# Performance work log

Hardware: AMD Instinct MI355X
Metric: run time of the kernel (lower is better)

Reference implementation:

```python
import jax, jax.numpy as jnp
import numpy as np

B, T, F = 32, 500, 640   # batch, encoder frames, encoder feature dim
H = 640                  # prediction-net LSTM hidden
J = 640                  # joint dim
V = 1024                 # vocab size
BLANK = 0                # blank_id


def setup_inputs() -> dict:
    key = jax.random.key(0)
    ks = jax.random.split(key, 8)
    s = 0.02
    return {
        "tn_output": jax.random.normal(ks[0], (B, T, F), jnp.float32),
        "E": jax.random.normal(ks[1], (V, H), jnp.float32) * s,        # prediction-net embedding
        "W_ih": jax.random.normal(ks[2], (H, 4 * H), jnp.float32) * s,  # LSTM input weights
        "W_hh": jax.random.normal(ks[3], (H, 4 * H), jnp.float32) * s,  # LSTM recurrent weights
        "b_lstm": jnp.zeros((4 * H,), jnp.float32),
        "W_enc": jax.random.normal(ks[4], (F, J), jnp.float32) * s,     # joint: encoder projection
        "W_dec": jax.random.normal(ks[5], (H, J), jnp.float32) * s,     # joint: decoder projection
        "b_j": jnp.zeros((J,), jnp.float32),
        "W_out": jax.random.normal(ks[6], (J, V), jnp.float32) * s,     # joint: output projection
        "b_out": jnp.zeros((V,), jnp.float32),
    }


def _lstm_step(x, h, c, W_ih, W_hh, b):
    gates = x @ W_ih + h @ W_hh + b  # [B, 4H]
    i, f, g, o = jnp.split(gates, 4, axis=-1)
    c2 = jax.nn.sigmoid(f) * c + jax.nn.sigmoid(i) * jnp.tanh(g)
    h2 = jax.nn.sigmoid(o) * jnp.tanh(c2)
    return h2, c2


def _greedy_decode(tn_output, E, W_ih, W_hh, b_lstm, W_enc, W_dec, b_j, W_out, b_out):
    Bc = tn_output.shape[0]
    dt = tn_output.dtype
    tok0 = jnp.full((Bc,), BLANK, jnp.int32)
    h0 = jnp.zeros((Bc, H), dt)
    c0 = jnp.zeros((Bc, H), dt)
    # initial decoder call on blank token (hidden=None -> zeros)
    h1, c1 = _lstm_step(E[tok0], h0, c0, W_ih, W_hh, b_lstm)
    g0 = h1  # out_PN

    def step(carry, enc_t):
        h, c, g, last_tok, scores = carry
        # joint network + log_softmax (idempotent, applied once)
        logits = jnp.tanh(enc_t @ W_enc + g @ W_dec + b_j) @ W_out + b_out  # [B, V]
        logp = jax.nn.log_softmax(logits, axis=-1)
        tok = jnp.argmax(logp, axis=-1)                                     # [B]
        lp = jnp.take_along_axis(logp, tok[:, None], axis=1)[:, 0]          # logp_targets
        emit = tok != BLANK                                                 # [B] bool
        scores = scores + jnp.where(emit, lp, jnp.zeros_like(lp))
        new_tok = jnp.where(emit, tok.astype(jnp.int32), last_tok)
        # conditional decoder step: run LSTM on all rows, keep updates only where emit
        h2, c2 = _lstm_step(E[new_tok], h, c, W_ih, W_hh, b_lstm)
        m = emit[:, None]
        h = jnp.where(m, h2, h)
        c = jnp.where(m, c2, c)
        g = jnp.where(m, h2, g)
        out_tok = jnp.where(emit, tok.astype(jnp.int32), jnp.int32(BLANK))
        return (h, c, g, new_tok, scores), out_tok

    init = (h1, c1, g0, tok0, jnp.zeros((Bc,), dt))
    (_, _, _, _, scores), toks = jax.lax.scan(step, init, jnp.swapaxes(tn_output, 0, 1))
    return jnp.swapaxes(toks, 0, 1), scores  # [B,T] int tokens (BLANK = no emission), [B] logp scores


def reference(tn_output, E, W_ih, W_hh, b_lstm, W_enc, W_dec, b_j, W_out, b_out):
    toks, scores = _greedy_decode(tn_output, E, W_ih, W_hh, b_lstm, W_enc, W_dec, b_j, W_out, b_out)
    # original returns (predictions, mean of exp(logp_scores), None, None)
    return toks, jnp.exp(scores).mean()
```

## Files before the change

### kernel.cpp

```cpp
#include <hip/hip_runtime.h>
#include <math.h>

#define BB 32
#define TT 500
#define HH 640
#define VV 1024
#define NWG 100

typedef float f32x4 __attribute__((ext_vector_type(4)));
typedef float f32x2 __attribute__((ext_vector_type(2)));
typedef unsigned int u32x2 __attribute__((ext_vector_type(2)));


__device__ __forceinline__ float sigf(float x) { return 1.0f / (1.0f + expf(-x)); }

__device__ __forceinline__ unsigned int fkey(float x) {
    unsigned int u = __float_as_uint(x);
    return (u & 0x80000000u) ? ~u : (u | 0x80000000u);
}

__device__ __forceinline__ unsigned long long shflxor_u64(unsigned long long v, int m) {
    unsigned int lo = (unsigned int)v, hi = (unsigned int)(v >> 32);
    lo = (unsigned int)__shfl_xor((int)lo, m);
    hi = (unsigned int)__shfl_xor((int)hi, m);
    return ((unsigned long long)hi << 32) | lo;
}

__device__ __forceinline__ void stg1_sc(float* p, float v) {
    asm volatile("global_store_dword %0, %1, off sc0 sc1" :: "v"(p), "v"(v) : "memory");
}
__device__ __forceinline__ void stg4_sc(float* p, f32x4 v) {
    asm volatile("global_store_dwordx4 %0, %1, off sc0 sc1" :: "v"(p), "v"(v) : "memory");
}
__device__ __forceinline__ void stg2u_sc(unsigned long long* p, unsigned long long v) {
    u32x2 uv; uv.x = (unsigned int)v; uv.y = (unsigned int)(v >> 32);
    asm volatile("global_store_dwordx2 %0, %1, off sc0 sc1" :: "v"(p), "v"(uv) : "memory");
}

__device__ __forceinline__ void stage_rows(const float* src, float* dst) {
    f32x4 t0,t1,t2,t3,t4,t5,t6,t7,t8,t9,t10,t11,t12,t13,t14,t15,t16,t17,t18,t19;
    asm volatile(
        "global_load_dwordx4 %0,  %20, off sc0 sc1\n\t"
        "global_load_dwordx4 %1,  %20, off offset:16 sc0 sc1\n\t"
        "global_load_dwordx4 %2,  %20, off offset:32 sc0 sc1\n\t"
        "global_load_dwordx4 %3,  %20, off offset:48 sc0 sc1\n\t"
        "global_load_dwordx4 %4,  %20, off offset:64 sc0 sc1\n\t"
        "global_load_dwordx4 %5,  %20, off offset:80 sc0 sc1\n\t"
        "global_load_dwordx4 %6,  %20, off offset:96 sc0 sc1\n\t"
        "global_load_dwordx4 %7,  %20, off offset:112 sc0 sc1\n\t"
        "global_load_dwordx4 %8,  %20, off offset:128 sc0 sc1\n\t"
        "global_load_dwordx4 %9,  %20, off offset:144 sc0 sc1\n\t"
        "global_load_dwordx4 %10, %20, off offset:160 sc0 sc1\n\t"
        "global_load_dwordx4 %11, %20, off offset:176 sc0 sc1\n\t"
        "global_load_dwordx4 %12, %20, off offset:192 sc0 sc1\n\t"
        "global_load_dwordx4 %13, %20, off offset:208 sc0 sc1\n\t"
        "global_load_dwordx4 %14, %20, off offset:224 sc0 sc1\n\t"
        "global_load_dwordx4 %15, %20, off offset:240 sc0 sc1\n\t"
        "global_load_dwordx4 %16, %20, off offset:256 sc0 sc1\n\t"
        "global_load_dwordx4 %17, %20, off offset:272 sc0 sc1\n\t"
        "global_load_dwordx4 %18, %20, off offset:288 sc0 sc1\n\t"
        "global_load_dwordx4 %19, %20, off offset:304 sc0 sc1\n\t"
        "s_waitcnt vmcnt(0)"
        : "=&v"(t0),"=&v"(t1),"=&v"(t2),"=&v"(t3),"=&v"(t4),"=&v"(t5),"=&v"(t6),"=&v"(t7),
          "=&v"(t8),"=&v"(t9),"=&v"(t10),"=&v"(t11),"=&v"(t12),"=&v"(t13),"=&v"(t14),"=&v"(t15),
          "=&v"(t16),"=&v"(t17),"=&v"(t18),"=&v"(t19)
        : "v"(src) : "memory");
    f32x4* d = (f32x4*)dst;
    d[0]=t0; d[1]=t1; d[2]=t2; d[3]=t3; d[4]=t4; d[5]=t5; d[6]=t6; d[7]=t7;
    d[8]=t8; d[9]=t9; d[10]=t10; d[11]=t11; d[12]=t12; d[13]=t13; d[14]=t14;
    d[15]=t15; d[16]=t16; d[17]=t17; d[18]=t18; d[19]=t19;
}

__device__ __forceinline__ void gbar(unsigned int* arrive, unsigned int* release,
                                     int w, int tid, unsigned int k) {
    asm volatile("s_waitcnt vmcnt(0)" ::: "memory");
    __syncthreads();
    if (w == 0) {
        if (tid > 0 && tid < NWG)
            while (__hip_atomic_load(&arrive[tid * 32], __ATOMIC_RELAXED,
                                     __HIP_MEMORY_SCOPE_AGENT) < k)
                __builtin_amdgcn_s_sleep(2);
        __syncthreads();
        if (tid > 0 && tid < NWG)
            __hip_atomic_store(&release[tid * 32], k, __ATOMIC_RELAXED,
                               __HIP_MEMORY_SCOPE_AGENT);
    } else {
        if (tid == 0) {
            __hip_atomic_store(&arrive[w * 32], k, __ATOMIC_RELAXED,
                               __HIP_MEMORY_SCOPE_AGENT);
            while (__hip_atomic_load(&release[w * 32], __ATOMIC_RELAXED,
                                     __HIP_MEMORY_SCOPE_AGENT) < k)
                __builtin_amdgcn_s_sleep(2);
        }
        __syncthreads();
    }
}

__global__ __launch_bounds__(256) void gemm_bias_kernel(
    const float* __restrict__ A, const float* __restrict__ Bm,
    const float* __restrict__ bias, float* __restrict__ C,
    int M, int N, int K)
{
    __shared__ float As[16][65];
    __shared__ float Bs[16][64];
    int tid = threadIdx.x;
    int m0 = blockIdx.y * 64, n0 = blockIdx.x * 64;
    int ar = tid >> 2, ac = (tid & 3) * 4;
    int br4 = (tid >> 6) * 4, bc = tid & 63;
    int ty = tid >> 4, tx = tid & 15;
    float acc[4][4] = {};
    for (int k0 = 0; k0 < K; k0 += 16) {
        float4 av = *(const float4*)(A + (long)(m0 + ar) * K + k0 + ac);
        As[ac + 0][ar] = av.x; As[ac + 1][ar] = av.y;
        As[ac + 2][ar] = av.z; As[ac + 3][ar] = av.w;
#pragma unroll
        for (int i = 0; i < 4; ++i)
            Bs[br4 + i][bc] = Bm[(long)(k0 + br4 + i) * N + n0 + bc];
        __syncthreads();
#pragma unroll
        for (int kk = 0; kk < 16; ++kk) {
            float a[4], b[4];
#pragma unroll
            for (int i = 0; i < 4; ++i) a[i] = As[kk][ty * 4 + i];
#pragma unroll
            for (int j = 0; j < 4; ++j) b[j] = Bs[kk][tx * 4 + j];
#pragma unroll
            for (int i = 0; i < 4; ++i)
#pragma unroll
                for (int j = 0; j < 4; ++j)
                    acc[i][j] = fmaf(a[i], b[j], acc[i][j]);
        }
        __syncthreads();
    }
#pragma unroll
    for (int i = 0; i < 4; ++i)
#pragma unroll
        for (int j = 0; j < 4; ++j)
            C[(long)(m0 + ty * 4 + i) * N + n0 + tx * 4 + j] =
                acc[i][j] + bias[n0 + tx * 4 + j];
}

__global__ void transpose_cat_kernel(const float* __restrict__ Wdec,
                                     const float* __restrict__ Whh,
                                     float* __restrict__ WcatT)
{
    int c = blockIdx.x;
    const float* src; long stride;
    if (c < 640) { src = Wdec + c; stride = 640; }
    else         { src = Whh + (c - 640); stride = 2560; }
    for (int k = threadIdx.x; k < 640; k += 256)
        WcatT[(long)c * 640 + k] = src[(long)k * stride];
}

__global__ void transpose_out_kernel(const float* __restrict__ Wout,
                                     float* __restrict__ WoT)
{
    int v = blockIdx.x;
    for (int k = threadIdx.x; k < 640; k += 256)
        WoT[(long)v * 640 + k] = Wout[(long)k * 1024 + v];
}

__global__ void init_kernel(const float* __restrict__ EW, float* __restrict__ h,
                            float* __restrict__ c, float* __restrict__ scores,
                            unsigned int* __restrict__ arrive,
                            unsigned int* __restrict__ release,
                            unsigned long long* __restrict__ pmax,
                            float* __restrict__ psum)
{
    int tid = threadIdx.x;
    for (int j = tid; j < HH; j += 256) {
        float gi = EW[j], gg = EW[1280 + j], go = EW[1920 + j];
        float c1 = sigf(gi) * tanhf(gg);
        float h1 = sigf(go) * tanhf(c1);
        for (int b = 0; b < BB; ++b) { h[b * 640 + j] = h1; c[b * 640 + j] = c1; }
    }
    if (tid < 32) scores[tid] = 0.f;
    if (tid < NWG) { arrive[tid * 32] = 0u; release[tid * 32] = 0u; }
    for (int i = tid; i < 32 * 128; i += 256) { pmax[i] = 0ull; psum[i] = 0.f; }
}

extern __shared__ float lds[];

__global__ __launch_bounds__(256, 1) void decode_kernel(
    const float* __restrict__ ENC, const float* __restrict__ EW,
    const float* __restrict__ WcatT, const float* __restrict__ WoT,
    const float* __restrict__ bout,
    float* __restrict__ h, float* __restrict__ c,
    float* __restrict__ Tt, float* __restrict__ G,
    unsigned long long* __restrict__ pmax, float* __restrict__ psum,
    float* __restrict__ scores, float* __restrict__ out,
    unsigned int* arrive, unsigned int* release)
{
    float* S = lds;
    float* P = lds + 20608;
    __shared__ int s_tok, s_emit;

    int w = blockIdx.x, tid = threadIdx.x;

    int srow = ((tid >> 3) + w) & 31;
    int scol = (tid & 7) * 80;
    int sgl  = srow * 640 + scol;
    int sll  = srow * 644 + scol;

    int ks = tid >> 5, bg = (tid >> 2) & 7, cg = tid & 3;
    int b0 = bg * 4, c0 = cg * 8;
    int C0 = w * 32;
    const float* wbase = WcatT + ((long)(C0 + c0)) * 640 + ks * 80;

    int pb = tid >> 3, pk8 = (tid & 7) * 80;
    int V0 = w * 10 + (w < 24 ? w : 24);
    int nv = 10 + (w < 24 ? 1 : 0);

    float score = 0.f;
    unsigned int bk = 0;

    for (int t = 0; t < TT; ++t) {
        stage_rows(h + sgl, &S[sll]);
        __syncthreads();
        {
            const float* sb = &S[b0 * 644 + ks * 80];
            float acc[4][8] = {};
            for (int kk = 0; kk < 80; kk += 4) {
                float4 hv[4];
#pragma unroll
                for (int i = 0; i < 4; ++i)
                    hv[i] = *(const float4*)(sb + i * 644 + kk);
#pragma unroll
                for (int j = 0; j < 8; ++j) {
                    float4 wv = *(const float4*)(wbase + (long)j * 640 + kk);
#pragma unroll
                    for (int i = 0; i < 4; ++i) {
                        acc[i][j] = fmaf(hv[i].x, wv.x, acc[i][j]);
                        acc[i][j] = fmaf(hv[i].y, wv.y, acc[i][j]);
                        acc[i][j] = fmaf(hv[i].z, wv.z, acc[i][j]);
                        acc[i][j] = fmaf(hv[i].w, wv.w, acc[i][j]);
                    }
                }
            }
#pragma unroll
            for (int i = 0; i < 4; ++i) {
                float4 v0, v1;
                v0.x = acc[i][0]; v0.y = acc[i][1]; v0.z = acc[i][2]; v0.w = acc[i][3];
                v1.x = acc[i][4]; v1.y = acc[i][5]; v1.z = acc[i][6]; v1.w = acc[i][7];
                *(float4*)&P[ks * 1152 + (b0 + i) * 36 + c0]     = v0;
                *(float4*)&P[ks * 1152 + (b0 + i) * 36 + c0 + 4] = v1;
            }
        }
        __syncthreads();
        {
            int rb = tid >> 3, rc = (tid & 7) * 4;
            float r0 = 0.f, r1 = 0.f, r2 = 0.f, r3 = 0.f;
#pragma unroll
            for (int kr = 0; kr < 8; ++kr) {
                float4 pv = *(const float4*)&P[kr * 1152 + rb * 36 + rc];
                r0 += pv.x; r1 += pv.y; r2 += pv.z; r3 += pv.w;
            }
            int gc = C0 + rc;
            f32x4 ov;
            if (w < 20) {
                float4 ev = *(const float4*)&ENC[((long)rb * TT + t) * 640 + gc];
                ov.x = tanhf(ev.x + r0); ov.y = tanhf(ev.y + r1);
                ov.z = tanhf(ev.z + r2); ov.w = tanhf(ev.w + r3);
                stg4_sc(&Tt[rb * 640 + gc], ov);
            } else {
                ov.x = r0; ov.y = r1; ov.z = r2; ov.w = r3;
                stg4_sc(&G[rb * 2560 + gc - 640], ov);
            }
        }
        gbar(arrive, release, w, tid, ++bk);

        stage_rows(Tt + sgl, &S[sll]);
        __syncthreads();
        {
            const float* tb = &S[pb * 644 + pk8];
            unsigned long long best = 0ull; float sex = 0.f;
            for (int vi = 0; vi < nv; ++vi) {
                int v = V0 + vi;
                const float* wb = WoT + (long)v * 640 + pk8;
                float acc = 0.f;
                for (int kk = 0; kk < 80; kk += 4) {
                    float4 tv = *(const float4*)(tb + kk);
                    float4 wv = *(const float4*)(wb + kk);
                    acc = fmaf(tv.x, wv.x, acc);
                    acc = fmaf(tv.y, wv.y, acc);
                    acc = fmaf(tv.z, wv.z, acc);
                    acc = fmaf(tv.w, wv.w, acc);
                }
                acc += __shfl_xor(acc, 1);
                acc += __shfl_xor(acc, 2);
                acc += __shfl_xor(acc, 4);
                if ((tid & 7) == 0) {
                    float logit = acc + bout[v];
                    sex += expf(logit);
                    unsigned long long q =
                        ((unsigned long long)fkey(logit) << 32) | (unsigned int)(1023 - v);
                    if (q > best) best = q;
                }
            }
            if ((tid & 7) == 0) {
                stg2u_sc(pmax + pb * 128 + w, best);
                stg1_sc(psum + pb * 128 + w, sex);
            }
        }
        gbar(arrive, release, w, tid, ++bk);

        if (w < 32) {
            int b = w;
            if (tid < 64) {
                u32x2 m1, m2; float s1, s2;
                asm volatile(
                    "global_load_dwordx2 %0, %4, off sc0 sc1\n\t"
                    "global_load_dwordx2 %1, %5, off sc0 sc1\n\t"
                    "global_load_dword   %2, %6, off sc0 sc1\n\t"
                    "global_load_dword   %3, %7, off sc0 sc1\n\t"
                    "s_waitcnt vmcnt(0)"
                    : "=&v"(m1), "=&v"(m2), "=&v"(s1), "=&v"(s2)
                    : "v"(pmax + b * 128 + tid), "v"(pmax + b * 128 + 64 + tid),
                      "v"(psum + b * 128 + tid), "v"(psum + b * 128 + 64 + tid)
                    : "memory");
                unsigned long long ma = ((unsigned long long)m1.y << 32) | m1.x;
                unsigned long long mb = ((unsigned long long)m2.y << 32) | m2.x;
                if (mb > ma) ma = mb;
                float s = s1 + s2;
#pragma unroll
                for (int mask = 1; mask <= 32; mask <<= 1) {
                    unsigned long long o = shflxor_u64(ma, mask);
                    if (o > ma) ma = o;
                    s += __shfl_xor(s, mask);
                }
                if (tid == 0) {
                    int tok = 1023 - (int)(ma & 0xFFFFFFFFu);
                    unsigned int key = (unsigned int)(ma >> 32);
                    unsigned int u = (key & 0x80000000u) ? (key ^ 0x80000000u) : ~key;
                    float maxlogit = __uint_as_float(u);
                    int emit = (tok != 0);
                    out[b * TT + t] = (float)tok;
                    if (emit) score += maxlogit - logf(s);
                    s_tok = tok; s_emit = emit;
                }
            }
            __syncthreads();
            if (s_emit && tid < 160) {
                int j4 = tid * 4;
                const float* gb = G + b * 2560 + j4;
                f32x4 vi, vf, vg, vo;
                asm volatile(
                    "global_load_dwordx4 %0, %4, off sc0 sc1\n\t"
                    "global_load_dwordx4 %1, %5, off sc0 sc1\n\t"
                    "global_load_dwordx4 %2, %6, off sc0 sc1\n\t"
                    "global_load_dwordx4 %3, %7, off sc0 sc1\n\t"
                    "s_waitcnt vmcnt(0)"
                    : "=&v"(vi), "=&v"(vf), "=&v"(vg), "=&v"(vo)
                    : "v"(gb), "v"(gb + 640), "v"(gb + 1280), "v"(gb + 1920)
                    : "memory");
                const float* ew = EW + (long)s_tok * 2560 + j4;
                float4 ei = *(const float4*)(ew);
                float4 ef = *(const float4*)(ew + 640);
                float4 eg = *(const float4*)(ew + 1280);
                float4 eo = *(const float4*)(ew + 1920);
                float4 cv = *(const float4*)(c + b * 640 + j4);
                float4 cn; f32x4 hn;
                cn.x = sigf(vf.x + ef.x) * cv.x + sigf(vi.x + ei.x) * tanhf(vg.x + eg.x);
                cn.y = sigf(vf.y + ef.y) * cv.y + sigf(vi.y + ei.y) * tanhf(vg.y + eg.y);
                cn.z = sigf(vf.z + ef.z) * cv.z + sigf(vi.z + ei.z) * tanhf(vg.z + eg.z);
                cn.w = sigf(vf.w + ef.w) * cv.w + sigf(vi.w + ei.w) * tanhf(vg.w + eg.w);
                hn.x = sigf(vo.x + eo.x) * tanhf(cn.x);
                hn.y = sigf(vo.y + eo.y) * tanhf(cn.y);
                hn.z = sigf(vo.z + eo.z) * tanhf(cn.z);
                hn.w = sigf(vo.w + eo.w) * tanhf(cn.w);
                *(float4*)(c + b * 640 + j4) = cn;
                stg4_sc(h + b * 640 + j4, hn);
            }
        }
        gbar(arrive, release, w, tid, ++bk);
    }

    if (w < 32 && tid == 0)
        stg1_sc(scores + w, score);
    gbar(arrive, release, w, tid, ++bk);

    if (w == 0 && tid == 0) {
        f32x4 s0,s1,s2,s3,s4,s5,s6,s7;
        asm volatile(
            "global_load_dwordx4 %0, %8, off sc0 sc1\n\t"
            "global_load_dwordx4 %1, %8, off offset:16 sc0 sc1\n\t"
            "global_load_dwordx4 %2, %8, off offset:32 sc0 sc1\n\t"
            "global_load_dwordx4 %3, %8, off offset:48 sc0 sc1\n\t"
            "global_load_dwordx4 %4, %8, off offset:64 sc0 sc1\n\t"
            "global_load_dwordx4 %5, %8, off offset:80 sc0 sc1\n\t"
            "global_load_dwordx4 %6, %8, off offset:96 sc0 sc1\n\t"
            "global_load_dwordx4 %7, %8, off offset:112 sc0 sc1\n\t"
            "s_waitcnt vmcnt(0)"
            : "=&v"(s0),"=&v"(s1),"=&v"(s2),"=&v"(s3),
              "=&v"(s4),"=&v"(s5),"=&v"(s6),"=&v"(s7)
            : "v"(scores) : "memory");
        float sum = expf(s0.x)+expf(s0.y)+expf(s0.z)+expf(s0.w)
                  + expf(s1.x)+expf(s1.y)+expf(s1.z)+expf(s1.w)
                  + expf(s2.x)+expf(s2.y)+expf(s2.z)+expf(s2.w)
                  + expf(s3.x)+expf(s3.y)+expf(s3.z)+expf(s3.w)
                  + expf(s4.x)+expf(s4.y)+expf(s4.z)+expf(s4.w)
                  + expf(s5.x)+expf(s5.y)+expf(s5.z)+expf(s5.w)
                  + expf(s6.x)+expf(s6.y)+expf(s6.z)+expf(s6.w)
                  + expf(s7.x)+expf(s7.y)+expf(s7.z)+expf(s7.w);
        out[16000] = sum / 32.0f;
    }
}

extern "C" void kernel_launch(void* const* d_in, const int* in_sizes, int n_in,
                              void* d_out, int out_size, void* d_ws, size_t ws_size,
                              hipStream_t stream)
{
    const float* X     = (const float*)d_in[0];
    const float* E     = (const float*)d_in[1];
    const float* W_ih  = (const float*)d_in[2];
    const float* W_hh  = (const float*)d_in[3];
    const float* b_l   = (const float*)d_in[4];
    const float* W_enc = (const float*)d_in[5];
    const float* W_dec = (const float*)d_in[6];
    const float* b_j   = (const float*)d_in[7];
    const float* W_out = (const float*)d_in[8];
    const float* b_out = (const float*)d_in[9];

    float* ws  = (float*)d_ws;
    float* ENC = ws;
    float* EW  = ws + 10240000;
    float* h   = ws + 12861440;
    float* c   = ws + 12881920;
    float* Tt  = ws + 12902400;
    float* G   = ws + 12922880;
    unsigned long long* pmax = (unsigned long long*)(ws + 13004800);
    float* psum   = ws + 13012992;
    float* scores = ws + 13017088;
    unsigned int* arrive  = (unsigned int*)(ws + 13017152);
    unsigned int* release = (unsigned int*)(ws + 13020352);
    float* WcatT  = ws + 13023552;
    float* WoT    = ws + 15071552;
    float* out = (float*)d_out;

    gemm_bias_kernel<<<dim3(10, 250), 256, 0, stream>>>(X, W_enc, b_j, ENC, 16000, 640, 640);
    gemm_bias_kernel<<<dim3(40, 16), 256, 0, stream>>>(E, W_ih, b_l, EW, 1024, 2560, 640);
    transpose_cat_kernel<<<3200, 256, 0, stream>>>(W_dec, W_hh, WcatT);
    transpose_out_kernel<<<1024, 256, 0, stream>>>(W_out, WoT);
    init_kernel<<<1, 256, 0, stream>>>(EW, h, c, scores, arrive, release, pmax, psum);

    void* args[] = {
        (void*)&ENC, (void*)&EW, (void*)&WcatT, (void*)&WoT,
        (void*)&b_out, (void*)&h, (void*)&c, (void*)&Tt, (void*)&G,
        (void*)&pmax, (void*)&psum, (void*)&scores, (void*)&out,
        (void*)&arrive, (void*)&release
    };
    hipLaunchCooperativeKernel((const void*)decode_kernel, dim3(NWG), dim3(256),
                               args, 119296, stream);
}
```

Baseline: 26.30 ms.

## Use per-timestep ring buffers for h and joint activations to allow cached loads

```diff
diff --git a/kernel.cpp b/kernel.cpp
--- a/kernel.cpp
+++ b/kernel.cpp
@@ -29,46 +29,15 @@
 __device__ __forceinline__ void stg1_sc(float* p, float v) {
     asm volatile("global_store_dword %0, %1, off sc0 sc1" :: "v"(p), "v"(v) : "memory");
 }
+__device__ __forceinline__ void stg2_sc(float* p, f32x2 v) {
+    asm volatile("global_store_dwordx2 %0, %1, off sc0 sc1" :: "v"(p), "v"(v) : "memory");
+}
 __device__ __forceinline__ void stg4_sc(float* p, f32x4 v) {
     asm volatile("global_store_dwordx4 %0, %1, off sc0 sc1" :: "v"(p), "v"(v) : "memory");
 }
 __device__ __forceinline__ void stg2u_sc(unsigned long long* p, unsigned long long v) {
     u32x2 uv; uv.x = (unsigned int)v; uv.y = (unsigned int)(v >> 32);
     asm volatile("global_store_dwordx2 %0, %1, off sc0 sc1" :: "v"(p), "v"(uv) : "memory");
-}
-
-__device__ __forceinline__ void stage_rows(const float* src, float* dst) {
-    f32x4 t0,t1,t2,t3,t4,t5,t6,t7,t8,t9,t10,t11,t12,t13,t14,t15,t16,t17,t18,t19;
-    asm volatile(
-        "global_load_dwordx4 %0,  %20, off sc0 sc1\n\t"
-        "global_load_dwordx4 %1,  %20, off offset:16 sc0 sc1\n\t"
-        "global_load_dwordx4 %2,  %20, off offset:32 sc0 sc1\n\t"
-        "global_load_dwordx4 %3,  %20, off offset:48 sc0 sc1\n\t"
-        "global_load_dwordx4 %4,  %20, off offset:64 sc0 sc1\n\t"
-        "global_load_dwordx4 %5,  %20, off offset:80 sc0 sc1\n\t"
-        "global_load_dwordx4 %6,  %20, off offset:96 sc0 sc1\n\t"
-        "global_load_dwordx4 %7,  %20, off offset:112 sc0 sc1\n\t"
-        "global_load_dwordx4 %8,  %20, off offset:128 sc0 sc1\n\t"
-        "global_load_dwordx4 %9,  %20, off offset:144 sc0 sc1\n\t"
-        "global_load_dwordx4 %10, %20, off offset:160 sc0 sc1\n\t"
-        "global_load_dwordx4 %11, %20, off offset:176 sc0 sc1\n\t"
-        "global_load_dwordx4 %12, %20, off offset:192 sc0 sc1\n\t"
-        "global_load_dwordx4 %13, %20, off offset:208 sc0 sc1\n\t"
-        "global_load_dwordx4 %14, %20, off offset:224 sc0 sc1\n\t"
-        "global_load_dwordx4 %15, %20, off offset:240 sc0 sc1\n\t"
-        "global_load_dwordx4 %16, %20, off offset:256 sc0 sc1\n\t"
-        "global_load_dwordx4 %17, %20, off offset:272 sc0 sc1\n\t"
-        "global_load_dwordx4 %18, %20, off offset:288 sc0 sc1\n\t"
-        "global_load_dwordx4 %19, %20, off offset:304 sc0 sc1\n\t"
-        "s_waitcnt vmcnt(0)"
-        : "=&v"(t0),"=&v"(t1),"=&v"(t2),"=&v"(t3),"=&v"(t4),"=&v"(t5),"=&v"(t6),"=&v"(t7),
-          "=&v"(t8),"=&v"(t9),"=&v"(t10),"=&v"(t11),"=&v"(t12),"=&v"(t13),"=&v"(t14),"=&v"(t15),
-          "=&v"(t16),"=&v"(t17),"=&v"(t18),"=&v"(t19)
-        : "v"(src) : "memory");
-    f32x4* d = (f32x4*)dst;
-    d[0]=t0; d[1]=t1; d[2]=t2; d[3]=t3; d[4]=t4; d[5]=t5; d[6]=t6; d[7]=t7;
-    d[8]=t8; d[9]=t9; d[10]=t10; d[11]=t11; d[12]=t12; d[13]=t13; d[14]=t14;
-    d[15]=t15; d[16]=t16; d[17]=t17; d[18]=t18; d[19]=t19;
 }
 
 __device__ __forceinline__ void gbar(unsigned int* arrive, unsigned int* release,
@@ -160,8 +129,8 @@
         WoT[(long)v * 640 + k] = Wout[(long)k * 1024 + v];
 }
 
-__global__ void init_kernel(const float* __restrict__ EW, float* __restrict__ h,
-                            float* __restrict__ c, float* __restrict__ scores,
+__global__ void init_kernel(const float* __restrict__ EW, float* __restrict__ hring,
+                            float* __restrict__ cst, float* __restrict__ scores,
                             unsigned int* __restrict__ arrive,
                             unsigned int* __restrict__ release,
                             unsigned long long* __restrict__ pmax,
@@ -172,7 +141,10 @@
         float gi = EW[j], gg = EW[1280 + j], go = EW[1920 + j];
         float c1 = sigf(gi) * tanhf(gg);
         float h1 = sigf(go) * tanhf(c1);
-        for (int b = 0; b < BB; ++b) { h[b * 640 + j] = h1; c[b * 640 + j] = c1; }
+        for (int b = 0; b < BB; ++b) {
+            hring[b * 640 + j] = h1;
+            cst[b * 640 + j] = c1;
+        }
     }
     if (tid < 32) scores[tid] = 0.f;
     if (tid < NWG) { arrive[tid * 32] = 0u; release[tid * 32] = 0u; }
@@ -185,8 +157,8 @@
     const float* __restrict__ ENC, const float* __restrict__ EW,
     const float* __restrict__ WcatT, const float* __restrict__ WoT,
     const float* __restrict__ bout,
-    float* __restrict__ h, float* __restrict__ c,
-    float* __restrict__ Tt, float* __restrict__ G,
+    float* __restrict__ hring, float* __restrict__ cst,
+    float* __restrict__ tring, float* __restrict__ G,
     unsigned long long* __restrict__ pmax, float* __restrict__ psum,
     float* __restrict__ scores, float* __restrict__ out,
     unsigned int* arrive, unsigned int* release)
@@ -197,8 +169,7 @@
 
     int w = blockIdx.x, tid = threadIdx.x;
 
-    int srow = ((tid >> 3) + w) & 31;
-    int scol = (tid & 7) * 80;
+    int srow = tid >> 3, scol = (tid & 7) * 80;
     int sgl  = srow * 640 + scol;
     int sll  = srow * 644 + scol;
 
@@ -215,7 +186,16 @@
     unsigned int bk = 0;
 
     for (int t = 0; t < TT; ++t) {
-        stage_rows(h + sgl, &S[sll]);
+        const float* hslot = hring + (long)t * 20480;
+        float* tslot = tring + (long)t * 20480;
+
+        {
+            const float* hsrc = hslot + sgl;
+            f32x4* d = (f32x4*)&S[sll];
+#pragma unroll
+            for (int i = 0; i < 20; ++i)
+                d[i] = *(const f32x4*)(hsrc + i * 4);
+        }
         __syncthreads();
         {
             const float* sb = &S[b0 * 644 + ks * 80];
@@ -261,7 +241,7 @@
                 float4 ev = *(const float4*)&ENC[((long)rb * TT + t) * 640 + gc];
                 ov.x = tanhf(ev.x + r0); ov.y = tanhf(ev.y + r1);
                 ov.z = tanhf(ev.z + r2); ov.w = tanhf(ev.w + r3);
-                stg4_sc(&Tt[rb * 640 + gc], ov);
+                stg4_sc(tslot + rb * 640 + gc, ov);
             } else {
                 ov.x = r0; ov.y = r1; ov.z = r2; ov.w = r3;
                 stg4_sc(&G[rb * 2560 + gc - 640], ov);
@@ -269,7 +249,13 @@
         }
         gbar(arrive, release, w, tid, ++bk);
 
-        stage_rows(Tt + sgl, &S[sll]);
+        {
+            const float* tsrc = tslot + sgl;
+            f32x4* d = (f32x4*)&S[sll];
+#pragma unroll
+            for (int i = 0; i < 20; ++i)
+                d[i] = *(const f32x4*)(tsrc + i * 4);
+        }
         __syncthreads();
         {
             const float* tb = &S[pb * 644 + pk8];
@@ -293,7 +279,7 @@
                     float logit = acc + bout[v];
                     sex += expf(logit);
                     unsigned long long q =
-                        ((unsigned long long)fkey(logit) << 32) | (unsigned int)(1023 - v);
+                        ((unsigned long long)fkey(logit) << 32) | (unsigned)(1023 - v);
                     if (q > best) best = q;
                 }
             }
@@ -340,36 +326,42 @@
                 }
             }
             __syncthreads();
-            if (s_emit && tid < 160) {
+            float* hnext = hring + (long)(t + 1) * 20480 + b * 640;
+            if (tid < 160) {
                 int j4 = tid * 4;
-                const float* gb = G + b * 2560 + j4;
-                f32x4 vi, vf, vg, vo;
-                asm volatile(
-                    "global_load_dwordx4 %0, %4, off sc0 sc1\n\t"
-                    "global_load_dwordx4 %1, %5, off sc0 sc1\n\t"
-                    "global_load_dwordx4 %2, %6, off sc0 sc1\n\t"
-                    "global_load_dwordx4 %3, %7, off sc0 sc1\n\t"
-                    "s_waitcnt vmcnt(0)"
-                    : "=&v"(vi), "=&v"(vf), "=&v"(vg), "=&v"(vo)
-                    : "v"(gb), "v"(gb + 640), "v"(gb + 1280), "v"(gb + 1920)
-                    : "memory");
-                const float* ew = EW + (long)s_tok * 2560 + j4;
-                float4 ei = *(const float4*)(ew);
-                float4 ef = *(const float4*)(ew + 640);
-                float4 eg = *(const float4*)(ew + 1280);
-                float4 eo = *(const float4*)(ew + 1920);
-                float4 cv = *(const float4*)(c + b * 640 + j4);
-                float4 cn; f32x4 hn;
-                cn.x = sigf(vf.x + ef.x) * cv.x + sigf(vi.x + ei.x) * tanhf(vg.x + eg.x);
-                cn.y = sigf(vf.y + ef.y) * cv.y + sigf(vi.y + ei.y) * tanhf(vg.y + eg.y);
-                cn.z = sigf(vf.z + ef.z) * cv.z + sigf(vi.z + ei.z) * tanhf(vg.z + eg.z);
-                cn.w = sigf(vf.w + ef.w) * cv.w + sigf(vi.w + ei.w) * tanhf(vg.w + eg.w);
-                hn.x = sigf(vo.x + eo.x) * tanhf(cn.x);
-                hn.y = sigf(vo.y + eo.y) * tanhf(cn.y);
-                hn.z = sigf(vo.z + eo.z) * tanhf(cn.z);
-                hn.w = sigf(vo.w + eo.w) * tanhf(cn.w);
-                *(float4*)(c + b * 640 + j4) = cn;
-                stg4_sc(h + b * 640 + j4, hn);
+                if (s_emit) {
+                    const float* gb = G + b * 2560 + j4;
+                    f32x4 vi, vf, vg, vo;
+                    asm volatile(
+                        "global_load_dwordx4 %0, %4, off sc0 sc1\n\t"
+                        "global_load_dwordx4 %1, %5, off sc0 sc1\n\t"
+                        "global_load_dwordx4 %2, %6, off sc0 sc1\n\t"
+                        "global_load_dwordx4 %3, %7, off sc0 sc1\n\t"
+                        "s_waitcnt vmcnt(0)"
+                        : "=&v"(vi), "=&v"(vf), "=&v"(vg), "=&v"(vo)
+                        : "v"(gb), "v"(gb + 640), "v"(gb + 1280), "v"(gb + 1920)
+                        : "memory");
+                    const float* ew = EW + (long)s_tok * 2560 + j4;
+                    float4 ei = *(const float4*)(ew);
+                    float4 ef = *(const float4*)(ew + 640);
+                    float4 eg = *(const float4*)(ew + 1280);
+                    float4 eo = *(const float4*)(ew + 1920);
+                    float4 cv = *(const float4*)(cst + b * 640 + j4);
+                    float4 cn; f32x4 hn;
+                    cn.x = sigf(vf.x + ef.x) * cv.x + sigf(vi.x + ei.x) * tanhf(vg.x + eg.x);
+                    cn.y = sigf(vf.y + ef.y) * cv.y + sigf(vi.y + ei.y) * tanhf(vg.y + eg.y);
+                    cn.z = sigf(vf.z + ef.z) * cv.z + sigf(vi.z + ei.z) * tanhf(vg.z + eg.z);
+                    cn.w = sigf(vf.w + ef.w) * cv.w + sigf(vi.w + ei.w) * tanhf(vg.w + eg.w);
+                    hn.x = sigf(vo.x + eo.x) * tanhf(cn.x);
+                    hn.y = sigf(vo.y + eo.y) * tanhf(cn.y);
+                    hn.z = sigf(vo.z + eo.z) * tanhf(cn.z);
+                    hn.w = sigf(vo.w + eo.w) * tanhf(cn.w);
+                    *(float4*)(cst + b * 640 + j4) = cn;
+                    stg4_sc(hnext + j4, hn);
+                } else {
+                    f32x4 hv = *(const f32x4*)(hring + (long)t * 20480 + b * 640 + j4);
+                    stg4_sc(hnext + j4, hv);
+                }
             }
         }
         gbar(arrive, release, w, tid, ++bk);
@@ -422,30 +414,30 @@
     const float* b_out = (const float*)d_in[9];
 
     float* ws  = (float*)d_ws;
-    float* ENC = ws;
-    float* EW  = ws + 10240000;
-    float* h   = ws + 12861440;
-    float* c   = ws + 12881920;
-    float* Tt  = ws + 12902400;
-    float* G   = ws + 12922880;
-    unsigned long long* pmax = (unsigned long long*)(ws + 13004800);
-    float* psum   = ws + 13012992;
-    float* scores = ws + 13017088;
-    unsigned int* arrive  = (unsigned int*)(ws + 13017152);
-    unsigned int* release = (unsigned int*)(ws + 13020352);
-    float* WcatT  = ws + 13023552;
-    float* WoT    = ws + 15071552;
+    float* ENC   = ws;
+    float* EW    = ws + 10240000;
+    float* hring = ws + 12861440;
+    float* tring = ws + 23121920;
+    float* cst   = ws + 33361920;
+    float* G     = ws + 33382400;
+    unsigned long long* pmax = (unsigned long long*)(ws + 33464320);
+    float* psum   = ws + 33472512;
+    float* scores = ws + 33476608;
+    unsigned int* arrive  = (unsigned int*)(ws + 33476672);
+    unsigned int* release = (unsigned int*)(ws + 33479872);
+    float* WcatT = ws + 33483072;
+    float* WoT   = ws + 35531072;
     float* out = (float*)d_out;
 
     gemm_bias_kernel<<<dim3(10, 250), 256, 0, stream>>>(X, W_enc, b_j, ENC, 16000, 640, 640);
     gemm_bias_kernel<<<dim3(40, 16), 256, 0, stream>>>(E, W_ih, b_l, EW, 1024, 2560, 640);
     transpose_cat_kernel<<<3200, 256, 0, stream>>>(W_dec, W_hh, WcatT);
     transpose_out_kernel<<<1024, 256, 0, stream>>>(W_out, WoT);
-    init_kernel<<<1, 256, 0, stream>>>(EW, h, c, scores, arrive, release, pmax, psum);
+    init_kernel<<<1, 256, 0, stream>>>(EW, hring, cst, scores, arrive, release, pmax, psum);
 
     void* args[] = {
-        (void*)&ENC, (void*)&EW, (void*)&WcatT, (void*)&WoT,
-        (void*)&b_out, (void*)&h, (void*)&c, (void*)&Tt, (void*)&G,
+        (void*)&ENC, (void*)&EW, (void*)&WcatT, (void*)&WoT, (void*)&b_out,
+        (void*)&hring, (void*)&cst, (void*)&tring, (void*)&G,
         (void*)&pmax, (void*)&psum, (void*)&scores, (void*)&out,
         (void*)&arrive, (void*)&release
     };
```

Result: faster. 25.63 ms (-2.6%).
